# Kernel tuning notes

Hardware: AMD Instinct MI355X
Metric: run time of the kernel (lower is better)

The kernel has to match this reference:

```python
import jax, jax.numpy as jnp
import numpy as np

S, V, L = 64, 16, 5            # hn_dim=(64,16), num_layers=5
ED, RD, TD = 16, 16, 64        # edge_dim, rbf_dim, t_dim
N, EL, EG, B = 16384, 131072, 262144, 64
FIN = 2 * S + RD + ED          # per-edge message input width
H = S + 2 * V                  # message output: scalar msg + 2 vector gates
CUT_L, CUT_G = 3.0, 10.0


def _ln(x, g, b, eps=1e-5):
    m = x.mean(-1, keepdims=True)
    var = ((x - m) ** 2).mean(-1, keepdims=True)
    return (x - m) / jnp.sqrt(var + eps) * g + b


def _seg_mean(x, idx, n):
    s = jax.ops.segment_sum(x, idx, num_segments=n)
    c = jax.ops.segment_sum(jnp.ones((x.shape[0], 1), x.dtype), idx, num_segments=n)
    return s / jnp.maximum(c, 1.0)


def _edge_geom(ei, pos, cutoff):
    src, tgt = ei[0], ei[1]
    r = pos[tgt] - pos[src]                       # [E,3]
    d = jnp.sqrt(jnp.clip((r * r).sum(-1), 1e-6))
    rn = r / d[:, None]
    centers = jnp.linspace(0.0, cutoff, RD)
    width = cutoff / RD
    env = jnp.where(d < cutoff, 0.5 * (jnp.cos(jnp.pi * d / cutoff) + 1.0), 0.0)
    rbf = jnp.exp(-0.5 * ((d[:, None] - centers) / width) ** 2) * env[:, None]
    return src, tgt, rn, rbf


def setup_inputs() -> dict:
    key = jax.random.key(0)
    ks = iter(jax.random.split(key, 32))
    nrm = lambda shp, sc=1.0: jax.random.normal(next(ks), shp, jnp.float32) * sc
    x = jax.random.randint(next(ks), (N, 3), 0, 16)
    t = nrm((B, TD))
    pos = nrm((N, 3))
    eil = jax.random.randint(next(ks), (2, EL), 0, N)
    eig = jax.random.randint(next(ks), (2, EG), 0, N)
    eal = jax.random.randint(next(ks), (EL,), 0, 5)
    eag = jax.random.randint(next(ks), (EG,), 0, 5)
    batch = jnp.sort(jax.random.randint(next(ks), (N,), 0, B))
    return dict(
        x=x, t=t, pos=pos,
        edge_index_local=eil, edge_index_global=eig,
        edge_attr_local=eal, edge_attr_global=eag, batch=batch,
        atom_emb=nrm((3, 16, S), 0.1),
        bond_emb=nrm((5, ED), 0.1),
        t_w1=nrm((TD, TD), TD ** -0.5), t_b1=jnp.zeros(TD),
        t_w2=nrm((TD, S), TD ** -0.5), t_b2=jnp.zeros(S),
        gnn_wm=nrm((L, 2, FIN, H), FIN ** -0.5), gnn_bm=jnp.zeros((L, 2, H)),
        gnn_wu=nrm((L, 2, S, S), S ** -0.5), gnn_bu=jnp.zeros((L, 2, S)),
        ln_g=jnp.ones((L, S)), ln_b=jnp.zeros((L, S)),
        head_dscore_w=nrm((S, 1), S ** -0.5),
        head_out_w=nrm((V, 1), V ** -0.5),
    )


def reference(x, t, pos, edge_index_local, edge_index_global, edge_attr_local,
              edge_attr_global, batch, atom_emb, bond_emb, t_w1, t_b1, t_w2,
              t_b2, gnn_wm, gnn_bm, gnn_wu, gnn_bu, ln_g, ln_b,
              head_dscore_w, head_out_w):
    n = x.shape[0]
    # AtomEncoder: sum of per-feature-column embeddings; + broadcast t-embedding
    s = atom_emb[0][x[:, 0]] + atom_emb[1][x[:, 1]] + atom_emb[2][x[:, 2]]
    temb = jax.nn.silu(jax.nn.silu(t @ t_w1 + t_b1) @ t_w2 + t_b2)
    s = s + temb[batch]
    v = jnp.zeros((n, 3, V), s.dtype)

    edge_sets = []
    for ei, ea, cut in ((edge_index_local, edge_attr_local, CUT_L),
                        (edge_index_global, edge_attr_global, CUT_G)):
        src, tgt, rn, rbf = _edge_geom(ei, pos, cut)
        edge_sets.append((src, tgt, rn, rbf, bond_emb[ea]))

    for i in range(L):
        for k, (src, tgt, rn, rbf, e) in enumerate(edge_sets):
            feat = jnp.concatenate([s[src], s[tgt], rbf, e], -1)       # [E,FIN]
            h = jax.nn.silu(feat @ gnn_wm[i, k] + gnn_bm[i, k])        # [E,H]
            ms, wv1, wv2 = h[:, :S], h[:, S:S + V], h[:, S + V:]
            vm = v[src] * wv1[:, None, :] + rn[:, :, None] * wv2[:, None, :]
            agg_s = _seg_mean(ms, tgt, n)                              # [N,S]
            agg_v = _seg_mean(vm.reshape(-1, 3 * V), tgt, n).reshape(n, 3, V)
            s = s + jax.nn.silu(agg_s @ gnn_wu[i, k] + gnn_bu[i, k])
            v = v + agg_v
        s = _ln(s, ln_g[i], ln_b[i])

    # ScoreHead (conservative=False)
    dsc = jax.nn.silu(s) @ head_dscore_w                               # [N,1]
    src, tgt = edge_index_global[0], edge_index_global[1]
    sr = (dsc[src] + dsc[tgt]) * (pos[src] - pos[tgt])                 # [E,3]
    sr = jax.ops.segment_sum(sr, tgt, num_segments=n)                  # [N,3]
    score = (v @ head_out_w)[..., 0] + sr                              # [N,3]
    return score
```

## Files before the change

kernel.cpp:

```cpp
#include <hip/hip_runtime.h>
#include <math.h>

#define Sdim 64
#define Vdim 16
#define NLAYER 5
#define EDdim 16
#define RDdim 16
#define TDdim 64
#define FINdim 160
#define Hdim 96
#define NVdim 48

typedef __attribute__((ext_vector_type(8))) short bf16x8;
typedef __attribute__((ext_vector_type(4))) float f32x4;

__device__ __forceinline__ float silu_f(float x) {
    return x / (1.0f + __expf(-x));
}

__device__ __forceinline__ unsigned short f2bf(float x) {
    union { float f; unsigned u; } v; v.f = x;
    unsigned r = v.u + 0x7fffu + ((v.u >> 16) & 1u);
    return (unsigned short)(r >> 16);
}

__device__ __forceinline__ float bf2f(unsigned short u) {
    union { unsigned u; float f; } v; v.u = (unsigned)u << 16;
    return v.f;
}

__global__ __launch_bounds__(256) void pack_kernel(
    const float* __restrict__ wm, const float* __restrict__ bemb,
    unsigned short* __restrict__ wp, unsigned short* __restrict__ bondbf)
{
    int idx = blockIdx.x * 256 + threadIdx.x;
    if (idx < 10 * FINdim * Hdim) {
        int ls = idx / (FINdim * Hdim), rem = idx % (FINdim * Hdim);
        int k = rem / Hdim, c = rem % Hdim;
        wp[(size_t)ls * FINdim * Hdim + ((size_t)(k >> 3) * Hdim + c) * 8 + (k & 7)] =
            f2bf(wm[idx]);
    } else if (idx < 10 * FINdim * Hdim + 80) {
        int i = idx - 10 * FINdim * Hdim;
        bondbf[i] = f2bf(bemb[i]);
    }
}

__global__ __launch_bounds__(64) void temb_kernel(
    const float* __restrict__ t, const float* __restrict__ w1, const float* __restrict__ b1,
    const float* __restrict__ w2, const float* __restrict__ b2, float* __restrict__ temb)
{
    int b = blockIdx.x, j = threadIdx.x;
    __shared__ float row[TDdim];
    __shared__ float hid[TDdim];
    row[j] = t[b * TDdim + j];
    __syncthreads();
    float h = b1[j];
    #pragma unroll 8
    for (int i = 0; i < TDdim; ++i) h = fmaf(row[i], w1[i * TDdim + j], h);
    h = silu_f(h);
    hid[j] = h;
    __syncthreads();
    float o = b2[j];
    #pragma unroll 8
    for (int i = 0; i < TDdim; ++i) o = fmaf(hid[i], w2[i * Sdim + j], o);
    temb[b * Sdim + j] = silu_f(o);
}

__global__ __launch_bounds__(256) void node_init_kernel(
    const int* __restrict__ x, const int* __restrict__ batch,
    const float* __restrict__ aemb, const float* __restrict__ temb,
    float* __restrict__ sfeat, unsigned short* __restrict__ sbf, int n)
{
    int idx = blockIdx.x * 256 + threadIdx.x;
    if (idx >= n * Sdim) return;
    int node = idx >> 6, j = idx & 63;
    int x0 = x[node * 3 + 0], x1 = x[node * 3 + 1], x2 = x[node * 3 + 2];
    float v = aemb[(0 * 16 + x0) * Sdim + j] + aemb[(16 + x1) * Sdim + j]
            + aemb[(32 + x2) * Sdim + j] + temb[batch[node] * Sdim + j];
    sfeat[idx] = v;
    sbf[idx]   = f2bf(v);
}

__global__ __launch_bounds__(256) void count_all_kernel(
    const int* __restrict__ eil, int EL,
    const int* __restrict__ eig, int EG,
    int* __restrict__ counts, int n)
{
    int idx = blockIdx.x * 256 + threadIdx.x;
    if (idx < EL) {
        atomicAdd(&counts[eil[EL + idx]], 1);
    } else if (idx < EL + EG) {
        int j = idx - EL;
        atomicAdd(&counts[n + eig[EG + j]], 1);
    }
}

__global__ __launch_bounds__(1024) void scan_kernel(
    const int* __restrict__ counts, int n2,
    int* __restrict__ rowStart, int* __restrict__ cursor)
{
    __shared__ int wsum[16];
    const int t = threadIdx.x;
    const int chunk = n2 >> 10;
    const int base = t * chunk;

    int4 c[8];
    const int4* c4 = reinterpret_cast<const int4*>(counts + base);
    #pragma unroll
    for (int i = 0; i < 8; ++i) c[i] = c4[i];

    int s = 0;
    #pragma unroll
    for (int i = 0; i < 8; ++i) s += c[i].x + c[i].y + c[i].z + c[i].w;

    const int lane = t & 63, w = t >> 6;
    int sc = s;
    #pragma unroll
    for (int off = 1; off < 64; off <<= 1) {
        int xv = __shfl_up(sc, off);
        if (lane >= off) sc += xv;
    }
    if (lane == 63) wsum[w] = sc;
    __syncthreads();
    int woff = 0;
    for (int i = 0; i < w; ++i) woff += wsum[i];
    int off = woff + sc - s;

    #pragma unroll
    for (int i = 0; i < 8; ++i) {
        int v0 = c[i].x, v1 = c[i].y, v2 = c[i].z, v3 = c[i].w;
        int o0 = off, o1 = o0 + v0, o2 = o1 + v1, o3 = o2 + v2;
        *reinterpret_cast<int4*>(rowStart + base + i * 4) = make_int4(o0, o1, o2, o3);
        *reinterpret_cast<int4*>(cursor   + base + i * 4) = make_int4(o0, o1, o2, o3);
        off = o3 + v3;
    }
    if (t == 1023) rowStart[n2] = off;
}

__global__ __launch_bounds__(256) void scatgeom_kernel(
    const int* __restrict__ eil, const int* __restrict__ eal, int EL,
    const int* __restrict__ eig, const int* __restrict__ eag, int EG,
    int* __restrict__ cursor, int n,
    const float* __restrict__ pos, const unsigned short* __restrict__ bondbf,
    int2* __restrict__ st2, float4* __restrict__ rn4,
    unsigned short* __restrict__ rbfb)
{
    int idx = blockIdx.x * 256 + threadIdx.x;
    if (idx >= EL + EG) return;
    int src, tgt, ea, cbase;
    float cutoff;
    if (idx < EL) {
        src = eil[idx]; tgt = eil[EL + idx]; ea = eal[idx];
        cbase = 0; cutoff = 3.0f;
    } else {
        int j = idx - EL;
        src = eig[j]; tgt = eig[EG + j]; ea = eag[j];
        cbase = n; cutoff = 10.0f;
    }
    int p = atomicAdd(&cursor[cbase + tgt], 1);
    st2[p] = make_int2(src, tgt);

    float rx = pos[3*tgt]-pos[3*src], ry = pos[3*tgt+1]-pos[3*src+1], rz = pos[3*tgt+2]-pos[3*src+2];
    float d = sqrtf(fmaxf(rx*rx + ry*ry + rz*rz, 1e-6f));
    float invd = 1.0f / d;
    rn4[p] = make_float4(rx*invd, ry*invd, rz*invd, d);
    float env = (d < cutoff) ? 0.5f * (__cosf(3.14159265358979f * d / cutoff) + 1.0f) : 0.0f;
    float invw = (float)RDdim / cutoff;
    unsigned int pk[8];
    #pragma unroll
    for (int i2 = 0; i2 < 8; ++i2) {
        float c0 = cutoff * ((float)(2*i2)     / 15.0f);
        float c1 = cutoff * ((float)(2*i2 + 1) / 15.0f);
        float t0 = (d - c0) * invw, t1 = (d - c1) * invw;
        unsigned short b0 = f2bf(__expf(-0.5f * t0 * t0) * env);
        unsigned short b1 = f2bf(__expf(-0.5f * t1 * t1) * env);
        pk[i2] = (unsigned)b0 | ((unsigned)b1 << 16);
    }
    uint4* o = reinterpret_cast<uint4*>(rbfb + (size_t)p * 32);
    o[0] = make_uint4(pk[0], pk[1], pk[2], pk[3]);
    o[1] = make_uint4(pk[4], pk[5], pk[6], pk[7]);
    const uint4* bp = reinterpret_cast<const uint4*>(bondbf + ea * EDdim);
    o[2] = bp[0];
    o[3] = bp[1];
}

__global__ __launch_bounds__(256) void edge_mlp_kernel(
    const unsigned short* __restrict__ sbf_in,
    const int2* __restrict__ st2,
    const unsigned short* __restrict__ rbfb,
    const unsigned short* __restrict__ wpk,
    const float* __restrict__ bg,
    unsigned short* __restrict__ hm,
    unsigned short* __restrict__ hv,
    int eOff)
{
    __shared__ __align__(16) unsigned short Wl[FINdim * Hdim];
    {
        const uint4* s4 = reinterpret_cast<const uint4*>(wpk);
        uint4* d4 = reinterpret_cast<uint4*>(Wl);
        for (int i = threadIdx.x; i < FINdim * Hdim / 8; i += 256) d4[i] = s4[i];
    }
    __syncthreads();

    const int lane = threadIdx.x & 63;
    const int wid  = threadIdx.x >> 6;
    const int l15 = lane & 15, l4 = lane >> 4;
    const int base0 = eOff + blockIdx.x * 128 + wid * 16;
    const int base1 = base0 + 64;

    const int2 st0 = st2[base0 + l15];
    const int2 st1 = st2[base1 + l15];
    bf16x8 a0[5], a1[5];
    {
        const unsigned short* sp = sbf_in + (size_t)st0.x * Sdim;
        const unsigned short* tp = sbf_in + (size_t)st0.y * Sdim;
        a0[0] = *reinterpret_cast<const bf16x8*>(sp + l4 * 8);
        a0[1] = *reinterpret_cast<const bf16x8*>(sp + 32 + l4 * 8);
        a0[2] = *reinterpret_cast<const bf16x8*>(tp + l4 * 8);
        a0[3] = *reinterpret_cast<const bf16x8*>(tp + 32 + l4 * 8);
        a0[4] = *reinterpret_cast<const bf16x8*>(rbfb + (size_t)(base0 + l15) * 32 + l4 * 8);
    }
    {
        const unsigned short* sp = sbf_in + (size_t)st1.x * Sdim;
        const unsigned short* tp = sbf_in + (size_t)st1.y * Sdim;
        a1[0] = *reinterpret_cast<const bf16x8*>(sp + l4 * 8);
        a1[1] = *reinterpret_cast<const bf16x8*>(sp + 32 + l4 * 8);
        a1[2] = *reinterpret_cast<const bf16x8*>(tp + l4 * 8);
        a1[3] = *reinterpret_cast<const bf16x8*>(tp + 32 + l4 * 8);
        a1[4] = *reinterpret_cast<const bf16x8*>(rbfb + (size_t)(base1 + l15) * 32 + l4 * 8);
    }

    f32x4 acc0[6], acc1[6];
    #pragma unroll
    for (int nt = 0; nt < 6; ++nt) {
        acc0[nt] = (f32x4){0.f, 0.f, 0.f, 0.f};
        acc1[nt] = (f32x4){0.f, 0.f, 0.f, 0.f};
    }
    #pragma unroll
    for (int kk = 0; kk < 5; ++kk) {
        #pragma unroll
        for (int nt = 0; nt < 6; ++nt) {
            bf16x8 b = *reinterpret_cast<const bf16x8*>(
                Wl + ((size_t)(kk * 4 + l4) * Hdim + nt * 16 + l15) * 8);
            acc0[nt] = __builtin_amdgcn_mfma_f32_16x16x32_bf16(a0[kk], b, acc0[nt], 0, 0, 0);
            acc1[nt] = __builtin_amdgcn_mfma_f32_16x16x32_bf16(a1[kk], b, acc1[nt], 0, 0, 0);
        }
    }

    #pragma unroll
    for (int nt = 0; nt < 6; ++nt) {
        const float bs = bg[nt * 16 + l15];
        #pragma unroll
        for (int r = 0; r < 4; ++r) {
            const int e0 = base0 + l4 * 4 + r;
            const int e1 = base1 + l4 * 4 + r;
            const unsigned short h0 = f2bf(silu_f(acc0[nt][r] + bs));
            const unsigned short h1 = f2bf(silu_f(acc1[nt][r] + bs));
            if (nt < 4) {
                hm[(size_t)e0 * 64 + nt * 16 + l15] = h0;
                hm[(size_t)e1 * 64 + nt * 16 + l15] = h1;
            } else {
                hv[(size_t)e0 * 32 + (nt - 4) * 16 + l15] = h0;
                hv[(size_t)e1 * 32 + (nt - 4) * 16 + l15] = h1;
            }
        }
    }
}

__global__ __launch_bounds__(64) void node_agg_kernel(
    const float* __restrict__ s_in, float* __restrict__ s_out,
    unsigned short* __restrict__ sbf_out,
    const float* __restrict__ v_in, float* __restrict__ v_out,
    const int* __restrict__ rowStart, const int2* __restrict__ st2,
    const float* __restrict__ rn4f,
    const unsigned short* __restrict__ hm, const unsigned short* __restrict__ hv,
    const float* __restrict__ wu, const float* __restrict__ bu,
    const float* __restrict__ lng, const float* __restrict__ lnb,
    int do_ln, int v_zero,
    int do_head, const float* __restrict__ wd, const float* __restrict__ wo,
    float* __restrict__ dsc, float* __restrict__ out)
{
    const int node = blockIdx.x;
    const int lane = threadIdx.x;
    const int l15 = lane & 15, dd = lane >> 4;
    const int lo = rowStart[node], hi = rowStart[node + 1];

    float msum0 = 0.0f, msum1 = 0.0f, vsum0 = 0.0f, vsum1 = 0.0f;
    int e = lo;
    for (; e + 1 < hi; e += 2) {
        msum0 += bf2f(hm[(size_t)e * 64 + lane]);
        msum1 += bf2f(hm[(size_t)(e + 1) * 64 + lane]);
        if (lane < NVdim) {
            float wv1a = bf2f(hv[(size_t)e * 32 + l15]);
            float wv2a = bf2f(hv[(size_t)e * 32 + 16 + l15]);
            float rnda = rn4f[(size_t)e * 4 + dd];
            float wv1b = bf2f(hv[(size_t)(e + 1) * 32 + l15]);
            float wv2b = bf2f(hv[(size_t)(e + 1) * 32 + 16 + l15]);
            float rndb = rn4f[(size_t)(e + 1) * 4 + dd];
            vsum0 = fmaf(rnda, wv2a, vsum0);
            vsum1 = fmaf(rndb, wv2b, vsum1);
            if (!v_zero) {
                float vva = v_in[(size_t)st2[e].x * NVdim + lane];
                float vvb = v_in[(size_t)st2[e + 1].x * NVdim + lane];
                vsum0 = fmaf(vva, wv1a, vsum0);
                vsum1 = fmaf(vvb, wv1b, vsum1);
            }
        }
    }
    if (e < hi) {
        msum0 += bf2f(hm[(size_t)e * 64 + lane]);
        if (lane < NVdim) {
            float wv1 = bf2f(hv[(size_t)e * 32 + l15]);
            float wv2 = bf2f(hv[(size_t)e * 32 + 16 + l15]);
            float rnd = rn4f[(size_t)e * 4 + dd];
            vsum0 = fmaf(rnd, wv2, vsum0);
            if (!v_zero) {
                float vv = v_in[(size_t)st2[e].x * NVdim + lane];
                vsum0 = fmaf(vv, wv1, vsum0);
            }
        }
    }
    float msum = msum0 + msum1;
    float vsum = vsum0 + vsum1;

    __shared__ float ag[64];
    const float ic = 1.0f / fmaxf((float)(hi - lo), 1.0f);
    ag[lane] = msum * ic;

    float dot = 0.0f;
    #pragma unroll 8
    for (int i = 0; i < Sdim; ++i) dot = fmaf(ag[i], wu[i * Sdim + lane], dot);
    float sn = s_in[(size_t)node * Sdim + lane] + silu_f(dot + bu[lane]);
    if (do_ln) {
        float mm = sn;
        #pragma unroll
        for (int off = 32; off >= 1; off >>= 1) mm += __shfl_xor(mm, off);
        mm *= (1.0f / 64.0f);
        float dv = sn - mm;
        float var = dv * dv;
        #pragma unroll
        for (int off = 32; off >= 1; off >>= 1) var += __shfl_xor(var, off);
        var *= (1.0f / 64.0f);
        sn = dv * rsqrtf(var + 1e-5f) * lng[lane] + lnb[lane];
    }
    s_out[(size_t)node * Sdim + lane]   = sn;
    sbf_out[(size_t)node * Sdim + lane] = f2bf(sn);
    float vnew = 0.0f;
    if (lane < NVdim) {
        float vprev = v_zero ? 0.0f : v_in[(size_t)node * NVdim + lane];
        vnew = vprev + vsum * ic;
        v_out[(size_t)node * NVdim + lane] = vnew;
    }

    if (do_head) {
        float val = silu_f(sn) * wd[lane];
        #pragma unroll
        for (int off = 32; off >= 1; off >>= 1) val += __shfl_xor(val, off);
        if (lane == 0) dsc[node] = val;
        float contrib = (lane < NVdim) ? vnew * wo[l15] : 0.0f;
        #pragma unroll
        for (int off = 1; off < 16; off <<= 1) contrib += __shfl_xor(contrib, off);
        if (lane < NVdim && l15 == 0) out[(size_t)node * 3 + dd] = contrib;
    }
}

__global__ __launch_bounds__(256) void head2_kernel(
    const float* __restrict__ dsc, const int* __restrict__ rsG,
    const int2* __restrict__ st2, const float4* __restrict__ rn4,
    float* __restrict__ out, int n)
{
    int t = blockIdx.x * 256 + threadIdx.x;
    if (t >= n) return;
    int lo = rsG[t], hi = rsG[t + 1];
    float dt = dsc[t];
    float ax = 0.f, ay = 0.f, az = 0.f;
    for (int e = lo; e < hi; ++e) {
        float w = dsc[st2[e].x] + dt;
        float4 rn = rn4[e];
        float wd_ = w * rn.w;
        ax -= wd_ * rn.x; ay -= wd_ * rn.y; az -= wd_ * rn.z;
    }
    out[3 * t + 0] += ax;
    out[3 * t + 1] += ay;
    out[3 * t + 2] += az;
}

extern "C" void kernel_launch(void* const* d_in, const int* in_sizes, int n_in,
                              void* d_out, int out_size, void* d_ws, size_t ws_size,
                              hipStream_t stream)
{
    const int*   x     = (const int*)d_in[0];
    const float* t     = (const float*)d_in[1];
    const float* pos   = (const float*)d_in[2];
    const int*   eil   = (const int*)d_in[3];
    const int*   eig   = (const int*)d_in[4];
    const int*   eal   = (const int*)d_in[5];
    const int*   eag   = (const int*)d_in[6];
    const int*   batch = (const int*)d_in[7];
    const float* aemb  = (const float*)d_in[8];
    const float* bemb  = (const float*)d_in[9];
    const float* t_w1  = (const float*)d_in[10];
    const float* t_b1  = (const float*)d_in[11];
    const float* t_w2  = (const float*)d_in[12];
    const float* t_b2  = (const float*)d_in[13];
    const float* wm    = (const float*)d_in[14];
    const float* bm    = (const float*)d_in[15];
    const float* wu    = (const float*)d_in[16];
    const float* bu    = (const float*)d_in[17];
    const float* lng   = (const float*)d_in[18];
    const float* lnb   = (const float*)d_in[19];
    const float* wd    = (const float*)d_in[20];
    const float* wo    = (const float*)d_in[21];

    const int n  = in_sizes[7];
    const int B  = in_sizes[1] / TDdim;
    const int EL = in_sizes[3] / 2;
    const int EG = in_sizes[4] / 2;
    const int ET = EL + EG;

    char* p = (char*)d_ws;
    auto alignup = [](char* q) { return (char*)(((size_t)q + 15) & ~(size_t)15); };

    float* temb = (float*)p;                 p += (size_t)B * Sdim * 4;
    float* dsc  = (float*)p;                 p += (size_t)n * 4;
    float* sA   = (float*)p;                 p += (size_t)n * Sdim * 4;
    float* sB   = (float*)p;                 p += (size_t)n * Sdim * 4;
    float* vA   = (float*)p;                 p += (size_t)n * NVdim * 4;
    float* vB   = (float*)p;                 p += (size_t)n * NVdim * 4;
    int* counts = (int*)p;                   p += (size_t)(2 * n) * 4;
    int* cursor = (int*)p;                   p += (size_t)(2 * n) * 4;
    int* rsAll  = (int*)p;                   p += (size_t)(2 * n + 4) * 4;
    p = alignup(p);
    int2* st2   = (int2*)p;                  p += (size_t)ET * 8;
    p = alignup(p);
    unsigned short* wp     = (unsigned short*)p;  p += (size_t)10 * FINdim * Hdim * 2;
    p = alignup(p);
    unsigned short* bondbf = (unsigned short*)p;  p += 96 * 2;
    p = alignup(p);
    unsigned short* sbfA   = (unsigned short*)p;  p += (size_t)n * Sdim * 2;
    unsigned short* sbfB   = (unsigned short*)p;  p += (size_t)n * Sdim * 2;
    p = alignup(p);
    float4* rn4 = (float4*)p;                p += (size_t)ET * 16;
    unsigned short* rbfb = (unsigned short*)p;    p += (size_t)ET * 32 * 2;
    p = alignup(p);
    unsigned short* hm = (unsigned short*)p; p += (size_t)ET * 64 * 2;
    unsigned short* hv = (unsigned short*)p; p += (size_t)ET * 32 * 2;

    float* out = (float*)d_out;

    pack_kernel<<<(10 * FINdim * Hdim + 80 + 255) / 256, 256, 0, stream>>>(wm, bemb, wp, bondbf);
    temb_kernel<<<B, 64, 0, stream>>>(t, t_w1, t_b1, t_w2, t_b2, temb);
    node_init_kernel<<<(n * Sdim + 255) / 256, 256, 0, stream>>>(x, batch, aemb, temb, sA, sbfA, n);

    hipMemsetAsync(counts, 0, (size_t)(2 * n) * sizeof(int), stream);
    count_all_kernel<<<(ET + 255) / 256, 256, 0, stream>>>(eil, EL, eig, EG, counts, n);
    scan_kernel<<<1, 1024, 0, stream>>>(counts, 2 * n, rsAll, cursor);
    scatgeom_kernel<<<(ET + 255) / 256, 256, 0, stream>>>(
        eil, eal, EL, eig, eag, EG, cursor, n, pos, bondbf, st2, rn4, rbfb);

    float* s_cur = sA; float* s_nxt = sB;
    float* v_cur = vA; float* v_nxt = vB;
    unsigned short* sb_cur = sbfA; unsigned short* sb_nxt = sbfB;

    for (int l = 0; l < NLAYER; ++l) {
        for (int k = 0; k < 2; ++k) {
            int ls = l * 2 + k;
            const unsigned short* wpk = wp + (size_t)ls * FINdim * Hdim;
            const float* bgk = bm + (size_t)ls * Hdim;
            const float* wuk = wu + (size_t)ls * Sdim * Sdim;
            const float* buk = bu + (size_t)ls * Sdim;
            const int E    = (k == 0) ? EL : EG;
            const int eOff = (k == 0) ? 0 : EL;
            const int* rsk = (k == 0) ? rsAll : rsAll + n;
            const int v_zero = (l == 0 && k == 0) ? 1 : 0;
            const int is_last = (l == NLAYER - 1 && k == 1) ? 1 : 0;

            edge_mlp_kernel<<<E / 128, 256, 0, stream>>>(
                sb_cur, st2, rbfb, wpk, bgk, hm, hv, eOff);
            node_agg_kernel<<<n, 64, 0, stream>>>(
                s_cur, s_nxt, sb_nxt, v_cur, v_nxt,
                rsk, st2, (const float*)rn4, hm, hv,
                wuk, buk, lng + (size_t)l * Sdim, lnb + (size_t)l * Sdim,
                (k == 1) ? 1 : 0, v_zero,
                is_last, wd, wo, dsc, out);

            float* tmp = s_cur; s_cur = s_nxt; s_nxt = tmp;
            tmp = v_cur; v_cur = v_nxt; v_nxt = tmp;
            unsigned short* tb = sb_cur; sb_cur = sb_nxt; sb_nxt = tb;
        }
    }

    head2_kernel<<<(n + 255) / 256, 256, 0, stream>>>(dsc, rsAll + n, st2, rn4, out, n);
}
```

Baseline: 606.3 us.

## Split node aggregation edges across four wavefronts and fold counts memset into pack

The node aggregation kernel now runs 256 threads per node. Four wavefronts each sum a strided quarter of the incoming edges, reduce the partial sums through shared memory, and split the 64x64 update matvec four ways before wave 0 finishes the LayerNorm and head. The aim is more memory-level parallelism per node for the gather-heavy reduction, at the cost of extra barriers and idle waves in the tail. Separately, zeroing the edge counts moves into the pack kernel, which removes the hipMemsetAsync call.

```diff
diff --git a/kernel.cpp b/kernel.cpp
--- a/kernel.cpp
+++ b/kernel.cpp
@@ -31,9 +31,11 @@
 
 __global__ __launch_bounds__(256) void pack_kernel(
     const float* __restrict__ wm, const float* __restrict__ bemb,
-    unsigned short* __restrict__ wp, unsigned short* __restrict__ bondbf)
+    unsigned short* __restrict__ wp, unsigned short* __restrict__ bondbf,
+    int* __restrict__ counts, int n2)
 {
     int idx = blockIdx.x * 256 + threadIdx.x;
+    if (idx < n2) counts[idx] = 0;
     if (idx < 10 * FINdim * Hdim) {
         int ls = idx / (FINdim * Hdim), rem = idx % (FINdim * Hdim);
         int k = rem / Hdim, c = rem % Hdim;
@@ -267,7 +269,7 @@
     }
 }
 
-__global__ __launch_bounds__(64) void node_agg_kernel(
+__global__ __launch_bounds__(256) void node_agg_kernel(
     const float* __restrict__ s_in, float* __restrict__ s_out,
     unsigned short* __restrict__ sbf_out,
     const float* __restrict__ v_in, float* __restrict__ v_out,
@@ -281,86 +283,86 @@
     float* __restrict__ dsc, float* __restrict__ out)
 {
     const int node = blockIdx.x;
-    const int lane = threadIdx.x;
+    const int tid  = threadIdx.x;
+    const int lane = tid & 63;
+    const int w    = tid >> 6;
     const int l15 = lane & 15, dd = lane >> 4;
     const int lo = rowStart[node], hi = rowStart[node + 1];
 
-    float msum0 = 0.0f, msum1 = 0.0f, vsum0 = 0.0f, vsum1 = 0.0f;
-    int e = lo;
-    for (; e + 1 < hi; e += 2) {
-        msum0 += bf2f(hm[(size_t)e * 64 + lane]);
-        msum1 += bf2f(hm[(size_t)(e + 1) * 64 + lane]);
-        if (lane < NVdim) {
-            float wv1a = bf2f(hv[(size_t)e * 32 + l15]);
-            float wv2a = bf2f(hv[(size_t)e * 32 + 16 + l15]);
-            float rnda = rn4f[(size_t)e * 4 + dd];
-            float wv1b = bf2f(hv[(size_t)(e + 1) * 32 + l15]);
-            float wv2b = bf2f(hv[(size_t)(e + 1) * 32 + 16 + l15]);
-            float rndb = rn4f[(size_t)(e + 1) * 4 + dd];
-            vsum0 = fmaf(rnda, wv2a, vsum0);
-            vsum1 = fmaf(rndb, wv2b, vsum1);
-            if (!v_zero) {
-                float vva = v_in[(size_t)st2[e].x * NVdim + lane];
-                float vvb = v_in[(size_t)st2[e + 1].x * NVdim + lane];
-                vsum0 = fmaf(vva, wv1a, vsum0);
-                vsum1 = fmaf(vvb, wv1b, vsum1);
-            }
-        }
-    }
-    if (e < hi) {
-        msum0 += bf2f(hm[(size_t)e * 64 + lane]);
+    float msum = 0.0f, vsum = 0.0f;
+    for (int e = lo + w; e < hi; e += 4) {
+        msum += bf2f(hm[(size_t)e * 64 + lane]);
         if (lane < NVdim) {
             float wv1 = bf2f(hv[(size_t)e * 32 + l15]);
             float wv2 = bf2f(hv[(size_t)e * 32 + 16 + l15]);
             float rnd = rn4f[(size_t)e * 4 + dd];
-            vsum0 = fmaf(rnd, wv2, vsum0);
+            vsum = fmaf(rnd, wv2, vsum);
             if (!v_zero) {
                 float vv = v_in[(size_t)st2[e].x * NVdim + lane];
-                vsum0 = fmaf(vv, wv1, vsum0);
+                vsum = fmaf(vv, wv1, vsum);
             }
         }
     }
-    float msum = msum0 + msum1;
-    float vsum = vsum0 + vsum1;
-
-    __shared__ float ag[64];
+
+    __shared__ float partm[4][64];
+    __shared__ float partv[4][48];
+    __shared__ float agS[64];
+    __shared__ float partd[4][64];
+
+    partm[w][lane] = msum;
+    if (lane < NVdim) partv[w][lane] = vsum;
+    __syncthreads();
+
     const float ic = 1.0f / fmaxf((float)(hi - lo), 1.0f);
-    ag[lane] = msum * ic;
-
-    float dot = 0.0f;
-    #pragma unroll 8
-    for (int i = 0; i < Sdim; ++i) dot = fmaf(ag[i], wu[i * Sdim + lane], dot);
-    float sn = s_in[(size_t)node * Sdim + lane] + silu_f(dot + bu[lane]);
-    if (do_ln) {
-        float mm = sn;
+    if (tid < 64)
+        agS[tid] = (partm[0][tid] + partm[1][tid] + partm[2][tid] + partm[3][tid]) * ic;
+    __syncthreads();
+
+    {
+        float dp = 0.0f;
         #pragma unroll
-        for (int off = 32; off >= 1; off >>= 1) mm += __shfl_xor(mm, off);
-        mm *= (1.0f / 64.0f);
-        float dv = sn - mm;
-        float var = dv * dv;
-        #pragma unroll
-        for (int off = 32; off >= 1; off >>= 1) var += __shfl_xor(var, off);
-        var *= (1.0f / 64.0f);
-        sn = dv * rsqrtf(var + 1e-5f) * lng[lane] + lnb[lane];
-    }
-    s_out[(size_t)node * Sdim + lane]   = sn;
-    sbf_out[(size_t)node * Sdim + lane] = f2bf(sn);
-    float vnew = 0.0f;
-    if (lane < NVdim) {
-        float vprev = v_zero ? 0.0f : v_in[(size_t)node * NVdim + lane];
-        vnew = vprev + vsum * ic;
-        v_out[(size_t)node * NVdim + lane] = vnew;
-    }
-
-    if (do_head) {
-        float val = silu_f(sn) * wd[lane];
-        #pragma unroll
-        for (int off = 32; off >= 1; off >>= 1) val += __shfl_xor(val, off);
-        if (lane == 0) dsc[node] = val;
-        float contrib = (lane < NVdim) ? vnew * wo[l15] : 0.0f;
-        #pragma unroll
-        for (int off = 1; off < 16; off <<= 1) contrib += __shfl_xor(contrib, off);
-        if (lane < NVdim && l15 == 0) out[(size_t)node * 3 + dd] = contrib;
+        for (int i = 0; i < 16; ++i) {
+            int ii = w * 16 + i;
+            dp = fmaf(agS[ii], wu[ii * Sdim + lane], dp);
+        }
+        partd[w][lane] = dp;
+    }
+    __syncthreads();
+
+    if (w == 0) {
+        float dot = partd[0][lane] + partd[1][lane] + partd[2][lane] + partd[3][lane];
+        float sn = s_in[(size_t)node * Sdim + lane] + silu_f(dot + bu[lane]);
+        if (do_ln) {
+            float mm = sn;
+            #pragma unroll
+            for (int off = 32; off >= 1; off >>= 1) mm += __shfl_xor(mm, off);
+            mm *= (1.0f / 64.0f);
+            float dv = sn - mm;
+            float var = dv * dv;
+            #pragma unroll
+            for (int off = 32; off >= 1; off >>= 1) var += __shfl_xor(var, off);
+            var *= (1.0f / 64.0f);
+            sn = dv * rsqrtf(var + 1e-5f) * lng[lane] + lnb[lane];
+        }
+        s_out[(size_t)node * Sdim + lane]   = sn;
+        sbf_out[(size_t)node * Sdim + lane] = f2bf(sn);
+        float vnew = 0.0f;
+        if (lane < NVdim) {
+            float vtot = (partv[0][lane] + partv[1][lane] + partv[2][lane] + partv[3][lane]) * ic;
+            float vprev = v_zero ? 0.0f : v_in[(size_t)node * NVdim + lane];
+            vnew = vprev + vtot;
+            v_out[(size_t)node * NVdim + lane] = vnew;
+        }
+        if (do_head) {
+            float val = silu_f(sn) * wd[lane];
+            #pragma unroll
+            for (int off = 32; off >= 1; off >>= 1) val += __shfl_xor(val, off);
+            if (lane == 0) dsc[node] = val;
+            float contrib = (lane < NVdim) ? vnew * wo[l15] : 0.0f;
+            #pragma unroll
+            for (int off = 1; off < 16; off <<= 1) contrib += __shfl_xor(contrib, off);
+            if (lane < NVdim && l15 == 0) out[(size_t)node * 3 + dd] = contrib;
+        }
     }
 }
 
@@ -448,11 +450,11 @@
 
     float* out = (float*)d_out;
 
-    pack_kernel<<<(10 * FINdim * Hdim + 80 + 255) / 256, 256, 0, stream>>>(wm, bemb, wp, bondbf);
+    pack_kernel<<<(10 * FINdim * Hdim + 80 + 255) / 256, 256, 0, stream>>>(
+        wm, bemb, wp, bondbf, counts, 2 * n);
     temb_kernel<<<B, 64, 0, stream>>>(t, t_w1, t_b1, t_w2, t_b2, temb);
     node_init_kernel<<<(n * Sdim + 255) / 256, 256, 0, stream>>>(x, batch, aemb, temb, sA, sbfA, n);
 
-    hipMemsetAsync(counts, 0, (size_t)(2 * n) * sizeof(int), stream);
     count_all_kernel<<<(ET + 255) / 256, 256, 0, stream>>>(eil, EL, eig, EG, counts, n);
     scan_kernel<<<1, 1024, 0, stream>>>(counts, 2 * n, rsAll, cursor);
     scatgeom_kernel<<<(ET + 255) / 256, 256, 0, stream>>>(
@@ -477,7 +479,7 @@
 
             edge_mlp_kernel<<<E / 128, 256, 0, stream>>>(
                 sb_cur, st2, rbfb, wpk, bgk, hm, hv, eOff);
-            node_agg_kernel<<<n, 64, 0, stream>>>(
+            node_agg_kernel<<<n, 256, 0, stream>>>(
                 s_cur, s_nxt, sb_nxt, v_cur, v_nxt,
                 rsk, st2, (const float*)rn4, hm, hv,
                 wuk, buk, lng + (size_t)l * Sdim, lnb + (size_t)l * Sdim,
```

New measurement: 755.6 us. +24.6%, slower.
